# Kernel tuning notes

Measured on AMD Instinct MI355X. Metric: run time of the kernel, lower is better.

## Reference

```python
import jax, jax.numpy as jnp
import numpy as np

N, E = 20000, 320000
NF, EF, GF = 74, 12, 128


def setup_inputs() -> dict:
    key = jax.random.key(0)
    it = iter(jax.random.split(key, 48))
    nrm = lambda shape, s=1.0: jax.random.normal(next(it), shape, jnp.float32) * s
    W = lambda shape: nrm(shape, 0.05)
    d = {}
    d["node_feats"] = nrm((N, NF))
    d["edge_feats"] = nrm((E, EF))
    for k in (1, 2, 3):
        d[f"pn{k}_w"] = W((NF, GF)); d[f"pn{k}_b"] = W((GF,))
        d[f"pe1{k}_w"] = W((NF + EF, GF)); d[f"pe1{k}_b"] = W((GF,))
        d[f"pe2{k}_w"] = W((2 * GF, 1)); d[f"pe2{k}_b"] = W((1,))
        d[f"et{k}_w"] = W((GF, GF)); d[f"et{k}_b"] = W((GF,))
    d["mca_w"] = W((3 * GF, GF)); d["mca_b"] = W((GF,))
    d["mcn_w"] = W((3 * GF, GF)); d["mcn_b"] = W((GF,))
    d["gru_wih"] = W((GF, 3 * GF)); d["gru_whh"] = W((GF, 3 * GF))
    d["gru_bih"] = W((3 * GF,)); d["gru_bhh"] = W((3 * GF,))
    d["src"] = jax.random.randint(next(it), (E,), 0, N, dtype=jnp.int32)
    d["dst"] = jax.random.randint(next(it), (E,), 0, N, dtype=jnp.int32)
    return d


def _forward(node_feats, edge_feats,
             pn1_w, pn1_b, pn2_w, pn2_b, pn3_w, pn3_b,
             pe11_w, pe11_b, pe12_w, pe12_b, pe13_w, pe13_b,
             pe21_w, pe21_b, pe22_w, pe22_b, pe23_w, pe23_b,
             et1_w, et1_b, et2_w, et2_b, et3_w, et3_b,
             mca_w, mca_b, mcn_w, mcn_b,
             gru_wih, gru_whh, gru_bih, gru_bhh,
             src, dst):
    leaky = lambda x: jax.nn.leaky_relu(x, 0.01)
    n_nodes = node_feats.shape[0]
    # projected node features (3 parallel branches), [N, GF]
    hv = [leaky(node_feats @ w + b)
          for w, b in ((pn1_w, pn1_b), (pn2_w, pn2_b), (pn3_w, pn3_b))]
    # apply_edges1: cat(src node feats, raw edge feats) -> [E, NF+EF]
    he1 = jnp.concatenate([node_feats[src], edge_feats], axis=1)
    he1k = [leaky(he1 @ w + b)
            for w, b in ((pe11_w, pe11_b), (pe12_w, pe12_b), (pe13_w, pe13_b))]
    pe2 = ((pe21_w, pe21_b), (pe22_w, pe22_b), (pe23_w, pe23_b))
    et = ((et1_w, et1_b), (et2_w, et2_b), (et3_w, et3_b))

    def edge_softmax(lg):  # softmax over incoming edges per destination node
        m = jax.ops.segment_max(lg, dst, num_segments=n_nodes)
        m = jnp.where(jnp.isfinite(m), m, 0.0)  # guard empty segments
        e = jnp.exp(lg - m[dst])
        s = jax.ops.segment_sum(e, dst, num_segments=n_nodes)
        return e / s[dst]

    ctx = []
    for k in range(3):
        w2, b2 = pe2[k]
        # apply_edges2: cat(dst projected node feats, projected edge feats) -> logits [E,1]
        lg = leaky(jnp.concatenate([hv[k][dst], he1k[k]], axis=1) @ w2 + b2)
        tw, tb = et[k]
        msg = edge_softmax(lg) * (he1k[k] @ tw + tb)  # [E, GF]
        ctx.append(jax.nn.elu(jax.ops.segment_sum(msg, dst, num_segments=n_nodes)))
    context = jnp.concatenate(ctx, axis=1) @ mca_w + mca_b  # [N, GF]
    h = jnp.concatenate(hv, axis=1) @ mcn_w + mcn_b          # [N, GF]
    # torch GRUCell(context, h)
    gi = context @ gru_wih + gru_bih
    gh = h @ gru_whh + gru_bhh
    ir, iz, inn = jnp.split(gi, 3, axis=1)
    hr, hz, hn = jnp.split(gh, 3, axis=1)
    r = jax.nn.sigmoid(ir + hr)
    z = jax.nn.sigmoid(iz + hz)
    n = jnp.tanh(inn + r * hn)
    return jax.nn.relu((1.0 - z) * n + z * h)


def reference(node_feats, edge_feats,
              pn1_w, pn1_b, pn2_w, pn2_b, pn3_w, pn3_b,
              pe11_w, pe11_b, pe12_w, pe12_b, pe13_w, pe13_b,
              pe21_w, pe21_b, pe22_w, pe22_b, pe23_w, pe23_b,
              et1_w, et1_b, et2_w, et2_b, et3_w, et3_b,
              mca_w, mca_b, mcn_w, mcn_b,
              gru_wih, gru_whh, gru_bih, gru_bhh,
              src, dst):
    return _forward(node_feats, edge_feats,
                    pn1_w, pn1_b, pn2_w, pn2_b, pn3_w, pn3_b,
                    pe11_w, pe11_b, pe12_w, pe12_b, pe13_w, pe13_b,
                    pe21_w, pe21_b, pe22_w, pe22_b, pe23_w, pe23_b,
                    et1_w, et1_b, et2_w, et2_b, et3_w, et3_b,
                    mca_w, mca_b, mcn_w, mcn_b,
                    gru_wih, gru_whh, gru_bih, gru_bhh,
                    src, dst)
```

## Files before the change

kernel.cpp:

```cpp
#include <hip/hip_runtime.h>
#include <hip/hip_bf16.h>
#include <math.h>

#define NN 20000
#define EE 320000
#define NFD 74
#define EFD 12

__device__ __forceinline__ float leakyf(float x) { return x > 0.f ? x : 0.01f * x; }
__device__ __forceinline__ float b2f(unsigned short u) {
    union { unsigned int i; float f; } x; x.i = ((unsigned int)u) << 16; return x.f;
}
__device__ __forceinline__ unsigned short f2b(float f) {
    __hip_bfloat16 h = __float2bfloat16(f);
    return *(unsigned short*)&h;
}

typedef __bf16 v8bf __attribute__((ext_vector_type(8)));
typedef float v4f __attribute__((ext_vector_type(4)));
typedef unsigned short us8v __attribute__((ext_vector_type(8)));
union FragU { v8bf v; ushort4 h[2]; };

struct GJob {
    const float* A; const float* B; const float* bias; float* C; const int* cnt;
    int a_off; int c_off; unsigned short* ph;
};

template <int ACT>
__global__ __launch_bounds__(256) void gemm_mfma(
    GJob j0, GJob j1, GJob j2,
    int lda, int ldb, int ldc, int nrows, int K, int M, int split)
{
    GJob jb = (blockIdx.y == 0) ? j0 : ((blockIdx.y == 1) ? j1 : j2);
    const int tiles_m = M >> 7;
    const int tn = blockIdx.x / tiles_m;
    const int tm = blockIdx.x % tiles_m;
    const int n0 = tn << 7, m0 = tm << 7;
    __shared__ __align__(16) unsigned short As[128][40];
    __shared__ __align__(16) unsigned short Bt[128][40];
    const int tid = threadIdx.x;
    const int w = tid >> 6, l = tid & 63;
    const int wr = (w >> 1) * 64, wc = (w & 1) * 64;
    const int fr = l & 15, fg = l >> 4;

    v4f acc[4][4];
#pragma unroll
    for (int ri = 0; ri < 4; ri++)
#pragma unroll
        for (int ci = 0; ci < 4; ci++) {
            acc[ri][ci][0] = 0.f; acc[ri][ci][1] = 0.f;
            acc[ri][ci][2] = 0.f; acc[ri][ci][3] = 0.f;
        }

    for (int k0 = 0; k0 < K; k0 += 32) {
        {
            const int row = tid >> 1, ks = (tid & 1) << 4;
            const int grow = n0 + row;
            const bool rok = grow < nrows;
            const float* Ap = jb.A + (size_t)grow * lda + jb.a_off + k0 + ks;
            unsigned short* dstp = &As[row][ks];
#pragma unroll
            for (int r = 0; r < 16; r += 4) {
                const int gk = k0 + ks + r;
                float4 v = make_float4(0.f, 0.f, 0.f, 0.f);
                if (rok && gk + 3 < K) v = *(const float4*)(Ap + r);
                dstp[r + 0] = f2b(v.x); dstp[r + 1] = f2b(v.y);
                dstp[r + 2] = f2b(v.z); dstp[r + 3] = f2b(v.w);
            }
        }
        {
            const int kk = tid >> 3, cb = (tid & 7) << 4;
            const int gk = k0 + kk;
            const bool kok = gk < K;
            const float* Bp = jb.B + (size_t)gk * ldb + m0 + cb;
#pragma unroll
            for (int r = 0; r < 4; r++) {
                float4 v = make_float4(0.f, 0.f, 0.f, 0.f);
                if (kok) v = *(const float4*)(Bp + r * 4);
                const int c = cb + r * 4;
                Bt[c + 0][kk] = f2b(v.x); Bt[c + 1][kk] = f2b(v.y);
                Bt[c + 2][kk] = f2b(v.z); Bt[c + 3][kk] = f2b(v.w);
            }
        }
        __syncthreads();
        FragU fa[4], fb[4];
#pragma unroll
        for (int ri = 0; ri < 4; ri++) {
            const unsigned short* ap = &As[wr + ri * 16 + fr][0];
            fa[ri].h[0] = *(const ushort4*)(ap + fg * 4);
            fa[ri].h[1] = *(const ushort4*)(ap + 16 + fg * 4);
        }
#pragma unroll
        for (int ci = 0; ci < 4; ci++) {
            const unsigned short* bp = &Bt[wc + ci * 16 + fr][0];
            fb[ci].h[0] = *(const ushort4*)(bp + fg * 4);
            fb[ci].h[1] = *(const ushort4*)(bp + 16 + fg * 4);
        }
#pragma unroll
        for (int ri = 0; ri < 4; ri++)
#pragma unroll
            for (int ci = 0; ci < 4; ci++)
                acc[ri][ci] = __builtin_amdgcn_mfma_f32_16x16x32_bf16(
                    fa[ri].v, fb[ci].v, acc[ri][ci], 0, 0, 0);
        __syncthreads();
    }
#pragma unroll
    for (int ci = 0; ci < 4; ci++) {
        const int gcol = m0 + wc + ci * 16 + fr;
        const float bi = jb.bias[gcol];
        const int gcc = jb.c_off + gcol;
#pragma unroll
        for (int ri = 0; ri < 4; ri++) {
#pragma unroll
            for (int j = 0; j < 4; j++) {
                const int grow = n0 + wr + ri * 16 + fg * 4 + j;
                if (grow >= nrows) continue;
                float v = acc[ri][ci][j] + bi;
                if (ACT == 2) {
                    bool pos = jb.cnt[grow] > 0;
                    v = pos ? (v > 0.f ? v : (__expf(v) - 1.f)) : 0.f;
                }
                if (ACT == 3) {
                    if (gcc < split) v = leakyf(v);
                    else if (jb.ph) jb.ph[(size_t)grow * 384 + (gcc - split)] = f2b(v);
                }
                jb.C[(size_t)grow * ldc + gcc] = v;
            }
        }
    }
}

__global__ void k_pack(
    const float* __restrict__ pn0, const float* __restrict__ pn1, const float* __restrict__ pn2,
    const float* __restrict__ pb0, const float* __restrict__ pb1, const float* __restrict__ pb2,
    const float* __restrict__ pe0, const float* __restrict__ pe1, const float* __restrict__ pe2,
    const float* __restrict__ qb0, const float* __restrict__ qb1, const float* __restrict__ qb2,
    const float* __restrict__ wih, const float* __restrict__ whh,
    float* __restrict__ PK, float* __restrict__ PB, float* __restrict__ WG, float* __restrict__ Z512)
{
    int idx = blockIdx.x * 256 + threadIdx.x;
    const float* pnw[3] = {pn0, pn1, pn2};
    const float* pew[3] = {pe0, pe1, pe2};
    const float* pnb[3] = {pb0, pb1, pb2};
    const float* peb[3] = {qb0, qb1, qb2};
    if (idx < 131072) {
        int r = idx >> 9, c = idx & 511;
        float v;
        if (r < 128) v = (c < 384) ? wih[r * 384 + c] : 0.f;
        else {
            int rr = r - 128;
            if (c < 256) v = whh[rr * 384 + c];
            else if (c < 384) v = 0.f;
            else v = whh[rr * 384 + (c - 128)];
        }
        WG[idx] = v;
    } else if (idx < 131072 + 61440) {
        int t = idx - 131072;
        int r = t / 768, c = t - r * 768;
        int k = (c >> 7) % 3, cc = c & 127;
        PK[t] = (r < NFD) ? ((c < 384) ? pnw[k][r * 128 + cc] : pew[k][r * 128 + cc]) : 0.f;
    } else if (idx < 131072 + 61440 + 768) {
        int c = idx - (131072 + 61440);
        int k = (c >> 7) % 3, cc = c & 127;
        PB[c] = (c < 384) ? pnb[k][cc] : peb[k][cc];
    } else if (idx < 131072 + 61440 + 768 + 512) {
        Z512[idx - (131072 + 61440 + 768)] = 0.f;
    }
}

__global__ void k_prep(const float* __restrict__ nf, float* __restrict__ PA)
{
    int idx = blockIdx.x * 256 + threadIdx.x;
    if (idx < NN * 80) {
        int n = idx / 80, c = idx - n * 80;
        PA[idx] = (c < NFD) ? nf[n * NFD + c] : 0.f;
    }
}

__global__ void k_count(const int* __restrict__ dst, int* __restrict__ cnt)
{
    int e = blockIdx.x * 256 + threadIdx.x;
    if (e < EE) atomicAdd(&cnt[dst[e]], 1);
}

__global__ void k_off(const int* __restrict__ cnt, int* __restrict__ offs,
                      int* __restrict__ cur, int* __restrict__ total)
{
    int n = blockIdx.x * 256 + threadIdx.x;
    if (n < NN) {
        int c = cnt[n];
        int o = atomicAdd(total, c);
        offs[n] = o;
        cur[n] = o;
    }
}

__global__ void k_fill(const int* __restrict__ dst, const int* __restrict__ src,
                       const float* __restrict__ ef,
                       int* __restrict__ cur, int* __restrict__ csr_src,
                       float* __restrict__ EFC)
{
    int e = blockIdx.x * 256 + threadIdx.x;
    if (e < EE) {
        int p = atomicAdd(&cur[dst[e]], 1);
        csr_src[p] = src[e];
        const float4* s = (const float4*)(ef + (size_t)e * 12);
        float4* d = (float4*)(EFC + (size_t)p * 12);
        float4 v0 = s[0], v1 = s[1], v2 = s[2];
        d[0] = v0; d[1] = v1; d[2] = v2;
    }
}

__global__ __launch_bounds__(256) void k_fused(
    const float* __restrict__ HP,
    const unsigned short* __restrict__ PH,
    const float* __restrict__ EFC,
    const float* __restrict__ pw0, const float* __restrict__ pw1, const float* __restrict__ pw2,
    const float* __restrict__ v0, const float* __restrict__ v1, const float* __restrict__ v2,
    const float* __restrict__ b20, const float* __restrict__ b21, const float* __restrict__ b22,
    const int* __restrict__ csr_src,
    const int* __restrict__ offs, const int* __restrict__ cnt,
    float* __restrict__ AX)
{
    const int wid = blockIdx.x * 4 + (threadIdx.x >> 6);
    const int n = wid / 3;
    const int k = wid - n * 3;
    if (n >= NN) return;
    const int lane = threadIdx.x & 63;
    const int er = lane >> 4, cg = lane & 15;
    const int c8 = cg * 8;
    const float* pw = (k == 0) ? pw0 : (k == 1) ? pw1 : pw2;
    const float* vv = (k == 0) ? v0 : (k == 1) ? v1 : v2;
    const float b2 = ((k == 0) ? b20 : (k == 1) ? b21 : b22)[0];
    const float* We = pw + NFD * 128;

    const int o0 = offs[n];
    const int deg = cnt[n];
    float* arow = AX + (size_t)n * 384 + k * 128;
    if (deg == 0) {
        if (er == 0) {
            *(float4*)(arow + c8) = make_float4(0.f, 0.f, 0.f, 0.f);
            *(float4*)(arow + c8 + 4) = make_float4(0.f, 0.f, 0.f, 0.f);
        }
        return;
    }

    float4 wb0 = *(const float4*)(vv + 128 + c8);
    float4 wb1 = *(const float4*)(vv + 128 + c8 + 4);

    float qa;
    {
        float4 wa0 = *(const float4*)(vv + c8);
        float4 wa1 = *(const float4*)(vv + c8 + 4);
        const float* hr = HP + (size_t)n * 768 + k * 128;
        float4 h0 = *(const float4*)(hr + c8);
        float4 h1 = *(const float4*)(hr + c8 + 4);
        qa = h0.x * wa0.x + h0.y * wa0.y + h0.z * wa0.z + h0.w * wa0.w
           + h1.x * wa1.x + h1.y * wa1.y + h1.z * wa1.z + h1.w * wa1.w;
#pragma unroll
        for (int d = 1; d < 16; d <<= 1) qa += __shfl_xor(qa, d, 64);
    }

    const unsigned short* PHk = PH + (size_t)k * 128 + c8;

    int q0 = o0 + ((er < deg) ? er : (deg - 1));
    int sn0 = csr_src[q0];
    const float4* ep0 = (const float4*)(EFC + (size_t)q0 * 12);
    float4 e00 = ep0[0], e01 = ep0[1], e02 = ep0[2];
    int sn1 = sn0;
    float4 e10 = e00, e11 = e01, e12 = e02;
    if (deg > 4) {
        int p1 = 4 + er;
        int q1 = o0 + ((p1 < deg) ? p1 : (deg - 1));
        sn1 = csr_src[q1];
        const float4* ep1 = (const float4*)(EFC + (size_t)q1 * 12);
        e10 = ep1[0]; e11 = ep1[1]; e12 = ep1[2];
    }
    us8v px0 = *(const us8v*)(PHk + (size_t)sn0 * 384);

    float4 a0 = make_float4(0.f, 0.f, 0.f, 0.f);
    float4 a1 = make_float4(0.f, 0.f, 0.f, 0.f);
    float s = 0.f;

    for (int base = 0; base < deg; base += 4) {
        const bool on = (base + er) < deg;
        us8v px1 = px0;
        if (base + 4 < deg) px1 = *(const us8v*)(PHk + (size_t)sn1 * 384);
        int sn2 = sn1;
        float4 e20 = e10, e21 = e11, e22 = e12;
        if (base + 8 < deg) {
            int p2 = base + 8 + er;
            int q2 = o0 + ((p2 < deg) ? p2 : (deg - 1));
            sn2 = csr_src[q2];
            const float4* ep2 = (const float4*)(EFC + (size_t)q2 * 12);
            e20 = ep2[0]; e21 = ep2[1]; e22 = ep2[2];
        }
        float ef[12] = {e00.x, e00.y, e00.z, e00.w, e01.x, e01.y, e01.z, e01.w,
                        e02.x, e02.y, e02.z, e02.w};
        float4 x0 = make_float4(0.f, 0.f, 0.f, 0.f);
        float4 x1 = make_float4(0.f, 0.f, 0.f, 0.f);
#pragma unroll
        for (int j = 0; j < 12; j++) {
            float e = ef[j];
            float4 w0 = *(const float4*)(We + j * 128 + c8);
            float4 w1 = *(const float4*)(We + j * 128 + c8 + 4);
            x0.x += e * w0.x; x0.y += e * w0.y; x0.z += e * w0.z; x0.w += e * w0.w;
            x1.x += e * w1.x; x1.y += e * w1.y; x1.z += e * w1.z; x1.w += e * w1.w;
        }
        x0.x = leakyf(x0.x + b2f(px0[0])); x0.y = leakyf(x0.y + b2f(px0[1]));
        x0.z = leakyf(x0.z + b2f(px0[2])); x0.w = leakyf(x0.w + b2f(px0[3]));
        x1.x = leakyf(x1.x + b2f(px0[4])); x1.y = leakyf(x1.y + b2f(px0[5]));
        x1.z = leakyf(x1.z + b2f(px0[6])); x1.w = leakyf(x1.w + b2f(px0[7]));
        float dd = x0.x * wb0.x + x0.y * wb0.y + x0.z * wb0.z + x0.w * wb0.w
                 + x1.x * wb1.x + x1.y * wb1.y + x1.z * wb1.z + x1.w * wb1.w;
#pragma unroll
        for (int d = 1; d < 16; d <<= 1) dd += __shfl_xor(dd, d, 64);
        float ex = on ? __expf(leakyf(qa + dd + b2)) : 0.f;
        a0.x += ex * x0.x; a0.y += ex * x0.y; a0.z += ex * x0.z; a0.w += ex * x0.w;
        a1.x += ex * x1.x; a1.y += ex * x1.y; a1.z += ex * x1.z; a1.w += ex * x1.w;
        s += ex;
        px0 = px1; sn1 = sn2;
        e00 = e10; e01 = e11; e02 = e12;
        e10 = e20; e11 = e21; e12 = e22;
    }
#pragma unroll
    for (int d = 16; d < 64; d <<= 1) {
        a0.x += __shfl_xor(a0.x, d, 64); a0.y += __shfl_xor(a0.y, d, 64);
        a0.z += __shfl_xor(a0.z, d, 64); a0.w += __shfl_xor(a0.w, d, 64);
        a1.x += __shfl_xor(a1.x, d, 64); a1.y += __shfl_xor(a1.y, d, 64);
        a1.z += __shfl_xor(a1.z, d, 64); a1.w += __shfl_xor(a1.w, d, 64);
        s += __shfl_xor(s, d, 64);
    }
    if (er == 0) {
        float inv = 1.f / s;
        a0.x *= inv; a0.y *= inv; a0.z *= inv; a0.w *= inv;
        a1.x *= inv; a1.y *= inv; a1.z *= inv; a1.w *= inv;
        *(float4*)(arow + c8) = a0;
        *(float4*)(arow + c8 + 4) = a1;
    }
}

__global__ void k_gru2(const float* __restrict__ G, const float* __restrict__ X,
                       const float* __restrict__ bih, const float* __restrict__ bhh,
                       float* __restrict__ out)
{
    int idx = blockIdx.x * 256 + threadIdx.x;
    if (idx >= NN * 128) return;
    int n = idx >> 7, c = idx & 127;
    const float* g = G + (size_t)n * 512;
    float r = 1.f / (1.f + __expf(-(g[c] + bih[c] + bhh[c])));
    float z = 1.f / (1.f + __expf(-(g[128 + c] + bih[128 + c] + bhh[128 + c])));
    float nv = tanhf(g[256 + c] + bih[256 + c] + r * (g[384 + c] + bhh[256 + c]));
    float h = X[(size_t)n * 256 + 128 + c];
    float v = (1.f - z) * nv + z * h;
    out[idx] = v > 0.f ? v : 0.f;
}

extern "C" void kernel_launch(void* const* d_in, const int* in_sizes, int n_in,
                              void* d_out, int out_size, void* d_ws, size_t ws_size,
                              hipStream_t stream)
{
    const float* nf = (const float*)d_in[0];
    const float* ef = (const float*)d_in[1];
    const float *pn_w[3], *pn_b[3], *pe1_w[3], *pe1_b[3], *pe2_w[3], *pe2_b[3], *et_w[3], *et_b[3];
    for (int k = 0; k < 3; k++) {
        int b = 2 + k * 8;
        pn_w[k] = (const float*)d_in[b + 0]; pn_b[k] = (const float*)d_in[b + 1];
        pe1_w[k] = (const float*)d_in[b + 2]; pe1_b[k] = (const float*)d_in[b + 3];
        pe2_w[k] = (const float*)d_in[b + 4]; pe2_b[k] = (const float*)d_in[b + 5];
        et_w[k] = (const float*)d_in[b + 6]; et_b[k] = (const float*)d_in[b + 7];
    }
    const float* mca_w = (const float*)d_in[26]; const float* mca_b = (const float*)d_in[27];
    const float* mcn_w = (const float*)d_in[28]; const float* mcn_b = (const float*)d_in[29];
    const float* wih = (const float*)d_in[30]; const float* whh = (const float*)d_in[31];
    const float* bih = (const float*)d_in[32]; const float* bhh = (const float*)d_in[33];
    const int* src = (const int*)d_in[34];
    const int* dst = (const int*)d_in[35];

    float* W = (float*)d_ws;
    size_t o = 0;
    float* HP = W + o;   o += (size_t)NN * 768;
    float* AX = W + o;   o += (size_t)NN * 384;
    float* EFC = W + o;  o += (size_t)EE * 12;
    float* PK = W + o;   o += 80 * 768;
    float* PB = W + o;   o += 768;
    float* WG = W + o;   o += 256 * 512;
    float* Z512 = W + o; o += 512;
    unsigned short* PHu = (unsigned short*)(W + o); o += (size_t)NN * 192;
    int* cnt = (int*)(W + o);
    int* total = cnt + NN;
    int* offs = total + 1;
    int* cur = offs + NN;
    int* csr_src = cur + NN;
    size_t need = o * 4 + (size_t)(NN * 3 + 1 + EE) * 4;
    if (ws_size < need) return;

    float* PA = EFC;
    float* Xb = AX;
    float* Gb = HP;

    hipMemsetAsync(cnt, 0, (NN + 1) * sizeof(int), stream);

    dim3 blk(256);
    k_pack<<<757, blk, 0, stream>>>(
        pn_w[0], pn_w[1], pn_w[2], pn_b[0], pn_b[1], pn_b[2],
        pe1_w[0], pe1_w[1], pe1_w[2], pe1_b[0], pe1_b[1], pe1_b[2],
        wih, whh, PK, PB, WG, Z512);
    k_prep<<<(NN * 80 + 255) / 256, blk, 0, stream>>>(nf, PA);

    const int rt = (NN + 127) / 128;

    {
        GJob j = {PA, PK, PB, HP, nullptr, 0, 0, PHu};
        gemm_mfma<3><<<dim3(rt * 6, 1), blk, 0, stream>>>(j, j, j, 80, 768, 768, NN, 80, 768, 384);
    }

    k_count<<<(EE + 255) / 256, blk, 0, stream>>>(dst, cnt);
    k_off<<<(NN + 255) / 256, blk, 0, stream>>>(cnt, offs, cur, total);
    k_fill<<<(EE + 255) / 256, blk, 0, stream>>>(dst, src, ef, cur, csr_src, EFC);

    k_fused<<<dim3((NN * 3) / 4), blk, 0, stream>>>(HP, PHu, EFC,
        pe1_w[0], pe1_w[1], pe1_w[2], pe2_w[0], pe2_w[1], pe2_w[2],
        pe2_b[0], pe2_b[1], pe2_b[2], csr_src, offs, cnt, AX);

    {
        GJob j0 = {AX, et_w[0], et_b[0], HP, cnt, 0 * 128, 384 + 0 * 128, nullptr};
        GJob j1 = {AX, et_w[1], et_b[1], HP, cnt, 1 * 128, 384 + 1 * 128, nullptr};
        GJob j2 = {AX, et_w[2], et_b[2], HP, cnt, 2 * 128, 384 + 2 * 128, nullptr};
        gemm_mfma<2><<<dim3(rt, 3), blk, 0, stream>>>(j0, j1, j2, 384, 128, 768, NN, 128, 128, 0);
    }
    {
        GJob j0 = {HP, mca_w, mca_b, Xb, nullptr, 384, 0, nullptr};
        GJob j1 = {HP, mcn_w, mcn_b, Xb, nullptr, 0, 128, nullptr};
        gemm_mfma<0><<<dim3(rt, 2), blk, 0, stream>>>(j0, j1, j1, 768, 128, 256, NN, 384, 128, 0);
    }
    {
        GJob j = {Xb, WG, Z512, Gb, nullptr, 0, 0, nullptr};
        gemm_mfma<0><<<dim3(rt * 4, 1), blk, 0, stream>>>(j, j, j, 256, 512, 512, NN, 256, 512, 0);
    }

    k_gru2<<<(NN * 128 + 255) / 256, blk, 0, stream>>>(Gb, Xb, bih, bhh, (float*)d_out);
}
```

Measured before the change: 529.6 us.

## Store intermediates and pre-transposed weights as bf16 to halve GEMM traffic

All GEMM operands are now bf16. Weights are packed once into transposed bf16 layouts, and activations (HP, AX, X) are written as bf16 by their producers. This lets the GEMM tile loads become plain 16-byte copies with no fp32-to-bf16 conversion or transposed scatter into shared memory, and it halves intermediate memory traffic. The fused edge kernel reads the unified bf16 HP buffer and writes bf16 output. Its block mapping is also reordered by branch, and the workspace aliasing is reorganised. The cost is slightly more rounding in the intermediates and a larger pack kernel.

```diff
diff --git a/kernel.cpp b/kernel.cpp
--- a/kernel.cpp
+++ b/kernel.cpp
@@ -22,14 +22,18 @@
 union FragU { v8bf v; ushort4 h[2]; };
 
 struct GJob {
-    const float* A; const float* B; const float* bias; float* C; const int* cnt;
-    int a_off; int c_off; unsigned short* ph;
+    const unsigned short* A;
+    const unsigned short* B;
+    const float* bias;
+    float* C;
+    unsigned short* Ch;
+    const int* cnt;
+    int lda; int a_off; int ldc; int ldch; int c_off;
 };
 
 template <int ACT>
-__global__ __launch_bounds__(256) void gemm_mfma(
-    GJob j0, GJob j1, GJob j2,
-    int lda, int ldb, int ldc, int nrows, int K, int M, int split)
+__global__ __launch_bounds__(256) void gemm_bf(
+    GJob j0, GJob j1, GJob j2, int nrows, int K, int M, int split)
 {
     GJob jb = (blockIdx.y == 0) ? j0 : ((blockIdx.y == 1) ? j1 : j2);
     const int tiles_m = M >> 7;
@@ -37,7 +41,7 @@
     const int tm = blockIdx.x % tiles_m;
     const int n0 = tn << 7, m0 = tm << 7;
     __shared__ __align__(16) unsigned short As[128][40];
-    __shared__ __align__(16) unsigned short Bt[128][40];
+    __shared__ __align__(16) unsigned short Bs[128][40];
     const int tid = threadIdx.x;
     const int w = tid >> 6, l = tid & 63;
     const int wr = (w >> 1) * 64, wc = (w & 1) * 64;
@@ -52,35 +56,25 @@
             acc[ri][ci][2] = 0.f; acc[ri][ci][3] = 0.f;
         }
 
+    const int row = tid >> 1, half = tid & 1;
+
     for (int k0 = 0; k0 < K; k0 += 32) {
+        const int kb = k0 + half * 16;
+        const bool kok = kb < K;
         {
-            const int row = tid >> 1, ks = (tid & 1) << 4;
-            const int grow = n0 + row;
-            const bool rok = grow < nrows;
-            const float* Ap = jb.A + (size_t)grow * lda + jb.a_off + k0 + ks;
-            unsigned short* dstp = &As[row][ks];
-#pragma unroll
-            for (int r = 0; r < 16; r += 4) {
-                const int gk = k0 + ks + r;
-                float4 v = make_float4(0.f, 0.f, 0.f, 0.f);
-                if (rok && gk + 3 < K) v = *(const float4*)(Ap + r);
-                dstp[r + 0] = f2b(v.x); dstp[r + 1] = f2b(v.y);
-                dstp[r + 2] = f2b(v.z); dstp[r + 3] = f2b(v.w);
-            }
+            const bool rok = kok && (n0 + row) < nrows;
+            const unsigned short* Ap = jb.A + (size_t)(n0 + row) * jb.lda + jb.a_off + kb;
+            uint4 v0 = make_uint4(0, 0, 0, 0), v1 = v0;
+            if (rok) { v0 = *(const uint4*)Ap; v1 = *(const uint4*)(Ap + 8); }
+            *(uint4*)&As[row][half * 16] = v0;
+            *(uint4*)&As[row][half * 16 + 8] = v1;
         }
         {
-            const int kk = tid >> 3, cb = (tid & 7) << 4;
-            const int gk = k0 + kk;
-            const bool kok = gk < K;
-            const float* Bp = jb.B + (size_t)gk * ldb + m0 + cb;
-#pragma unroll
-            for (int r = 0; r < 4; r++) {
-                float4 v = make_float4(0.f, 0.f, 0.f, 0.f);
-                if (kok) v = *(const float4*)(Bp + r * 4);
-                const int c = cb + r * 4;
-                Bt[c + 0][kk] = f2b(v.x); Bt[c + 1][kk] = f2b(v.y);
-                Bt[c + 2][kk] = f2b(v.z); Bt[c + 3][kk] = f2b(v.w);
-            }
+            const unsigned short* Bp = jb.B + (size_t)(m0 + row) * K + kb;
+            uint4 v0 = make_uint4(0, 0, 0, 0), v1 = v0;
+            if (kok) { v0 = *(const uint4*)Bp; v1 = *(const uint4*)(Bp + 8); }
+            *(uint4*)&Bs[row][half * 16] = v0;
+            *(uint4*)&Bs[row][half * 16 + 8] = v1;
         }
         __syncthreads();
         FragU fa[4], fb[4];
@@ -92,7 +86,7 @@
         }
 #pragma unroll
         for (int ci = 0; ci < 4; ci++) {
-            const unsigned short* bp = &Bt[wc + ci * 16 + fr][0];
+            const unsigned short* bp = &Bs[wc + ci * 16 + fr][0];
             fb[ci].h[0] = *(const ushort4*)(bp + fg * 4);
             fb[ci].h[1] = *(const ushort4*)(bp + 16 + fg * 4);
         }
@@ -109,42 +103,57 @@
         const int gcol = m0 + wc + ci * 16 + fr;
         const float bi = jb.bias[gcol];
         const int gcc = jb.c_off + gcol;
+        const bool lk = (ACT == 3) && (gcc < split);
 #pragma unroll
         for (int ri = 0; ri < 4; ri++) {
 #pragma unroll
-            for (int j = 0; j < 4; j++) {
-                const int grow = n0 + wr + ri * 16 + fg * 4 + j;
+            for (int jj = 0; jj < 4; jj++) {
+                const int grow = n0 + wr + ri * 16 + fg * 4 + jj;
                 if (grow >= nrows) continue;
-                float v = acc[ri][ci][j] + bi;
+                float v = acc[ri][ci][jj] + bi;
                 if (ACT == 2) {
                     bool pos = jb.cnt[grow] > 0;
                     v = pos ? (v > 0.f ? v : (__expf(v) - 1.f)) : 0.f;
                 }
-                if (ACT == 3) {
-                    if (gcc < split) v = leakyf(v);
-                    else if (jb.ph) jb.ph[(size_t)grow * 384 + (gcc - split)] = f2b(v);
-                }
-                jb.C[(size_t)grow * ldc + gcc] = v;
+                if (ACT == 3 && lk) v = leakyf(v);
+                if (jb.C)  jb.C[(size_t)grow * jb.ldc + gcc] = v;
+                if (jb.Ch) jb.Ch[(size_t)grow * jb.ldch + gcc] = f2b(v);
             }
         }
     }
 }
 
+#define SZ_PKT 61440
+#define SZ_WGT 131072
+#define SZ_ETT 49152
+#define SZ_MCT 98304
 __global__ void k_pack(
     const float* __restrict__ pn0, const float* __restrict__ pn1, const float* __restrict__ pn2,
     const float* __restrict__ pb0, const float* __restrict__ pb1, const float* __restrict__ pb2,
     const float* __restrict__ pe0, const float* __restrict__ pe1, const float* __restrict__ pe2,
     const float* __restrict__ qb0, const float* __restrict__ qb1, const float* __restrict__ qb2,
     const float* __restrict__ wih, const float* __restrict__ whh,
-    float* __restrict__ PK, float* __restrict__ PB, float* __restrict__ WG, float* __restrict__ Z512)
+    const float* __restrict__ et0, const float* __restrict__ et1, const float* __restrict__ et2,
+    const float* __restrict__ mca, const float* __restrict__ mcn,
+    unsigned short* __restrict__ PKt, unsigned short* __restrict__ WGt,
+    unsigned short* __restrict__ ETt, unsigned short* __restrict__ MCt,
+    float* __restrict__ PB, float* __restrict__ Z512)
 {
     int idx = blockIdx.x * 256 + threadIdx.x;
     const float* pnw[3] = {pn0, pn1, pn2};
     const float* pew[3] = {pe0, pe1, pe2};
     const float* pnb[3] = {pb0, pb1, pb2};
     const float* peb[3] = {qb0, qb1, qb2};
-    if (idx < 131072) {
-        int r = idx >> 9, c = idx & 511;
+    const float* etw[3] = {et0, et1, et2};
+    if (idx < SZ_PKT) {
+        int c = idx / 80, r = idx - c * 80;
+        int k = (c >> 7) % 3, cc = c & 127;
+        float v = 0.f;
+        if (r < NFD) v = (c < 384) ? pnw[k][r * 128 + cc] : pew[k][r * 128 + cc];
+        PKt[idx] = f2b(v);
+    } else if (idx < SZ_PKT + SZ_WGT) {
+        int t = idx - SZ_PKT;
+        int c = t >> 8, r = t & 255;
         float v;
         if (r < 128) v = (c < 384) ? wih[r * 384 + c] : 0.f;
         else {
@@ -153,27 +162,32 @@
             else if (c < 384) v = 0.f;
             else v = whh[rr * 384 + (c - 128)];
         }
-        WG[idx] = v;
-    } else if (idx < 131072 + 61440) {
-        int t = idx - 131072;
-        int r = t / 768, c = t - r * 768;
-        int k = (c >> 7) % 3, cc = c & 127;
-        PK[t] = (r < NFD) ? ((c < 384) ? pnw[k][r * 128 + cc] : pew[k][r * 128 + cc]) : 0.f;
-    } else if (idx < 131072 + 61440 + 768) {
-        int c = idx - (131072 + 61440);
+        WGt[t] = f2b(v);
+    } else if (idx < SZ_PKT + SZ_WGT + SZ_ETT) {
+        int t = idx - (SZ_PKT + SZ_WGT);
+        int k = t / 16384, rem = t - k * 16384;
+        int c = rem >> 7, r = rem & 127;
+        ETt[t] = f2b(etw[k][r * 128 + c]);
+    } else if (idx < SZ_PKT + SZ_WGT + SZ_ETT + SZ_MCT) {
+        int t = idx - (SZ_PKT + SZ_WGT + SZ_ETT);
+        int m = t / 49152, rem = t - m * 49152;
+        int c = rem / 384, r = rem - c * 384;
+        MCt[t] = f2b((m == 0 ? mca : mcn)[r * 128 + c]);
+    } else if (idx < SZ_PKT + SZ_WGT + SZ_ETT + SZ_MCT + 768) {
+        int c = idx - (SZ_PKT + SZ_WGT + SZ_ETT + SZ_MCT);
         int k = (c >> 7) % 3, cc = c & 127;
         PB[c] = (c < 384) ? pnb[k][cc] : peb[k][cc];
-    } else if (idx < 131072 + 61440 + 768 + 512) {
-        Z512[idx - (131072 + 61440 + 768)] = 0.f;
-    }
-}
-
-__global__ void k_prep(const float* __restrict__ nf, float* __restrict__ PA)
+    } else if (idx < SZ_PKT + SZ_WGT + SZ_ETT + SZ_MCT + 768 + 512) {
+        Z512[idx - (SZ_PKT + SZ_WGT + SZ_ETT + SZ_MCT + 768)] = 0.f;
+    }
+}
+
+__global__ void k_prep(const float* __restrict__ nf, unsigned short* __restrict__ PA)
 {
     int idx = blockIdx.x * 256 + threadIdx.x;
     if (idx < NN * 80) {
         int n = idx / 80, c = idx - n * 80;
-        PA[idx] = (c < NFD) ? nf[n * NFD + c] : 0.f;
+        PA[idx] = f2b((c < NFD) ? nf[n * NFD + c] : 0.f);
     }
 }
 
@@ -212,20 +226,17 @@
 }
 
 __global__ __launch_bounds__(256) void k_fused(
-    const float* __restrict__ HP,
-    const unsigned short* __restrict__ PH,
+    const unsigned short* __restrict__ HPh,
     const float* __restrict__ EFC,
     const float* __restrict__ pw0, const float* __restrict__ pw1, const float* __restrict__ pw2,
     const float* __restrict__ v0, const float* __restrict__ v1, const float* __restrict__ v2,
     const float* __restrict__ b20, const float* __restrict__ b21, const float* __restrict__ b22,
     const int* __restrict__ csr_src,
     const int* __restrict__ offs, const int* __restrict__ cnt,
-    float* __restrict__ AX)
-{
-    const int wid = blockIdx.x * 4 + (threadIdx.x >> 6);
-    const int n = wid / 3;
-    const int k = wid - n * 3;
-    if (n >= NN) return;
+    unsigned short* __restrict__ AXh)
+{
+    const int k = blockIdx.x / (NN / 4);
+    const int n = (blockIdx.x - k * (NN / 4)) * 4 + (threadIdx.x >> 6);
     const int lane = threadIdx.x & 63;
     const int er = lane >> 4, cg = lane & 15;
     const int c8 = cg * 8;
@@ -236,11 +247,13 @@
 
     const int o0 = offs[n];
     const int deg = cnt[n];
-    float* arow = AX + (size_t)n * 384 + k * 128;
+    unsigned short* arow = AXh + (size_t)n * 384 + k * 128 + c8;
     if (deg == 0) {
         if (er == 0) {
-            *(float4*)(arow + c8) = make_float4(0.f, 0.f, 0.f, 0.f);
-            *(float4*)(arow + c8 + 4) = make_float4(0.f, 0.f, 0.f, 0.f);
+            us8v z;
+#pragma unroll
+            for (int i = 0; i < 8; i++) z[i] = 0;
+            *(us8v*)arow = z;
         }
         return;
     }
@@ -252,16 +265,14 @@
     {
         float4 wa0 = *(const float4*)(vv + c8);
         float4 wa1 = *(const float4*)(vv + c8 + 4);
-        const float* hr = HP + (size_t)n * 768 + k * 128;
-        float4 h0 = *(const float4*)(hr + c8);
-        float4 h1 = *(const float4*)(hr + c8 + 4);
-        qa = h0.x * wa0.x + h0.y * wa0.y + h0.z * wa0.z + h0.w * wa0.w
-           + h1.x * wa1.x + h1.y * wa1.y + h1.z * wa1.z + h1.w * wa1.w;
+        us8v h8 = *(const us8v*)(HPh + (size_t)n * 768 + k * 128 + c8);
+        qa = b2f(h8[0]) * wa0.x + b2f(h8[1]) * wa0.y + b2f(h8[2]) * wa0.z + b2f(h8[3]) * wa0.w
+           + b2f(h8[4]) * wa1.x + b2f(h8[5]) * wa1.y + b2f(h8[6]) * wa1.z + b2f(h8[7]) * wa1.w;
 #pragma unroll
         for (int d = 1; d < 16; d <<= 1) qa += __shfl_xor(qa, d, 64);
     }
 
-    const unsigned short* PHk = PH + (size_t)k * 128 + c8;
+    const unsigned short* PHk = HPh + 384 + (size_t)k * 128 + c8;
 
     int q0 = o0 + ((er < deg) ? er : (deg - 1));
     int sn0 = csr_src[q0];
@@ -276,7 +287,7 @@
         const float4* ep1 = (const float4*)(EFC + (size_t)q1 * 12);
         e10 = ep1[0]; e11 = ep1[1]; e12 = ep1[2];
     }
-    us8v px0 = *(const us8v*)(PHk + (size_t)sn0 * 384);
+    us8v px0 = *(const us8v*)(PHk + (size_t)sn0 * 768);
 
     float4 a0 = make_float4(0.f, 0.f, 0.f, 0.f);
     float4 a1 = make_float4(0.f, 0.f, 0.f, 0.f);
@@ -285,7 +296,7 @@
     for (int base = 0; base < deg; base += 4) {
         const bool on = (base + er) < deg;
         us8v px1 = px0;
-        if (base + 4 < deg) px1 = *(const us8v*)(PHk + (size_t)sn1 * 384);
+        if (base + 4 < deg) px1 = *(const us8v*)(PHk + (size_t)sn1 * 768);
         int sn2 = sn1;
         float4 e20 = e10, e21 = e11, e22 = e12;
         if (base + 8 < deg) {
@@ -333,10 +344,12 @@
     }
     if (er == 0) {
         float inv = 1.f / s;
-        a0.x *= inv; a0.y *= inv; a0.z *= inv; a0.w *= inv;
-        a1.x *= inv; a1.y *= inv; a1.z *= inv; a1.w *= inv;
-        *(float4*)(arow + c8) = a0;
-        *(float4*)(arow + c8 + 4) = a1;
+        us8v outv;
+        outv[0] = f2b(a0.x * inv); outv[1] = f2b(a0.y * inv);
+        outv[2] = f2b(a0.z * inv); outv[3] = f2b(a0.w * inv);
+        outv[4] = f2b(a1.x * inv); outv[5] = f2b(a1.y * inv);
+        outv[6] = f2b(a1.z * inv); outv[7] = f2b(a1.w * inv);
+        *(us8v*)arow = outv;
     }
 }
 
@@ -379,65 +392,70 @@
 
     float* W = (float*)d_ws;
     size_t o = 0;
-    float* HP = W + o;   o += (size_t)NN * 768;
-    float* AX = W + o;   o += (size_t)NN * 384;
-    float* EFC = W + o;  o += (size_t)EE * 12;
-    float* PK = W + o;   o += 80 * 768;
-    float* PB = W + o;   o += 768;
-    float* WG = W + o;   o += 256 * 512;
-    float* Z512 = W + o; o += 512;
-    unsigned short* PHu = (unsigned short*)(W + o); o += (size_t)NN * 192;
+    float* Xb = W + o;                                  o += (size_t)NN * 256;
+    unsigned short* HPh = (unsigned short*)(W + o);     o += (size_t)NN * 384;
+    unsigned short* Xh  = (unsigned short*)(W + o);     o += (size_t)NN * 128;
+    unsigned short* PKt = (unsigned short*)(W + o);     o += SZ_PKT / 2;
+    unsigned short* WGt = (unsigned short*)(W + o);     o += SZ_WGT / 2;
+    unsigned short* ETt = (unsigned short*)(W + o);     o += SZ_ETT / 2;
+    unsigned short* MCt = (unsigned short*)(W + o);     o += SZ_MCT / 2;
+    float* PB = W + o;                                  o += 768;
+    float* Z512 = W + o;                                o += 512;
     int* cnt = (int*)(W + o);
     int* total = cnt + NN;
     int* offs = total + 1;
     int* cur = offs + NN;
-    int* csr_src = cur + NN;
-    size_t need = o * 4 + (size_t)(NN * 3 + 1 + EE) * 4;
+    int* csr_src = cur + NN;                            o += (size_t)3 * NN + 1 + EE;
+    float* G = W + o;
+    unsigned short* AXh = (unsigned short*)G;
+    float* EFC = G + (size_t)NN * 192;
+    unsigned short* PA = (unsigned short*)EFC;
+    size_t gspan = (size_t)NN * 512;
+    size_t espan = (size_t)NN * 192 + (size_t)EE * 12;
+    o += (gspan > espan) ? gspan : espan;
+    size_t need = o * 4;
     if (ws_size < need) return;
 
-    float* PA = EFC;
-    float* Xb = AX;
-    float* Gb = HP;
-
     hipMemsetAsync(cnt, 0, (NN + 1) * sizeof(int), stream);
 
     dim3 blk(256);
-    k_pack<<<757, blk, 0, stream>>>(
+    k_pack<<<(SZ_PKT + SZ_WGT + SZ_ETT + SZ_MCT + 768 + 512 + 255) / 256, blk, 0, stream>>>(
         pn_w[0], pn_w[1], pn_w[2], pn_b[0], pn_b[1], pn_b[2],
         pe1_w[0], pe1_w[1], pe1_w[2], pe1_b[0], pe1_b[1], pe1_b[2],
-        wih, whh, PK, PB, WG, Z512);
+        wih, whh, et_w[0], et_w[1], et_w[2], mca_w, mcn_w,
+        PKt, WGt, ETt, MCt, PB, Z512);
     k_prep<<<(NN * 80 + 255) / 256, blk, 0, stream>>>(nf, PA);
 
     const int rt = (NN + 127) / 128;
 
     {
-        GJob j = {PA, PK, PB, HP, nullptr, 0, 0, PHu};
-        gemm_mfma<3><<<dim3(rt * 6, 1), blk, 0, stream>>>(j, j, j, 80, 768, 768, NN, 80, 768, 384);
+        GJob j = {PA, PKt, PB, nullptr, HPh, nullptr, 80, 0, 0, 768, 0};
+        gemm_bf<3><<<dim3(rt * 6, 1), blk, 0, stream>>>(j, j, j, NN, 80, 768, 384);
     }
 
     k_count<<<(EE + 255) / 256, blk, 0, stream>>>(dst, cnt);
     k_off<<<(NN + 255) / 256, blk, 0, stream>>>(cnt, offs, cur, total);
     k_fill<<<(EE + 255) / 256, blk, 0, stream>>>(dst, src, ef, cur, csr_src, EFC);
 
-    k_fused<<<dim3((NN * 3) / 4), blk, 0, stream>>>(HP, PHu, EFC,
+    k_fused<<<dim3((NN / 4) * 3), blk, 0, stream>>>(HPh, EFC,
         pe1_w[0], pe1_w[1], pe1_w[2], pe2_w[0], pe2_w[1], pe2_w[2],
-        pe2_b[0], pe2_b[1], pe2_b[2], csr_src, offs, cnt, AX);
+        pe2_b[0], pe2_b[1], pe2_b[2], csr_src, offs, cnt, AXh);
 
     {
-        GJob j0 = {AX, et_w[0], et_b[0], HP, cnt, 0 * 128, 384 + 0 * 128, nullptr};
-        GJob j1 = {AX, et_w[1], et_b[1], HP, cnt, 1 * 128, 384 + 1 * 128, nullptr};
-        GJob j2 = {AX, et_w[2], et_b[2], HP, cnt, 2 * 128, 384 + 2 * 128, nullptr};
-        gemm_mfma<2><<<dim3(rt, 3), blk, 0, stream>>>(j0, j1, j2, 384, 128, 768, NN, 128, 128, 0);
+        GJob j0 = {AXh, ETt,             et_b[0], nullptr, HPh, cnt, 384, 0,   0, 768, 384};
+        GJob j1 = {AXh, ETt + 16384,     et_b[1], nullptr, HPh, cnt, 384, 128, 0, 768, 512};
+        GJob j2 = {AXh, ETt + 32768,     et_b[2], nullptr, HPh, cnt, 384, 256, 0, 768, 640};
+        gemm_bf<2><<<dim3(rt, 3), blk, 0, stream>>>(j0, j1, j2, NN, 128, 128, 0);
     }
     {
-        GJob j0 = {HP, mca_w, mca_b, Xb, nullptr, 384, 0, nullptr};
-        GJob j1 = {HP, mcn_w, mcn_b, Xb, nullptr, 0, 128, nullptr};
-        gemm_mfma<0><<<dim3(rt, 2), blk, 0, stream>>>(j0, j1, j1, 768, 128, 256, NN, 384, 128, 0);
+        GJob j0 = {HPh, MCt,         mca_b, Xb, Xh, nullptr, 768, 384, 256, 256, 0};
+        GJob j1 = {HPh, MCt + 49152, mcn_b, Xb, Xh, nullptr, 768, 0,   256, 256, 128};
+        gemm_bf<0><<<dim3(rt, 2), blk, 0, stream>>>(j0, j1, j1, NN, 384, 128, 0);
     }
     {
-        GJob j = {Xb, WG, Z512, Gb, nullptr, 0, 0, nullptr};
-        gemm_mfma<0><<<dim3(rt * 4, 1), blk, 0, stream>>>(j, j, j, 256, 512, 512, NN, 256, 512, 0);
-    }
-
-    k_gru2<<<(NN * 128 + 255) / 256, blk, 0, stream>>>(Gb, Xb, bih, bhh, (float*)d_out);
-}
+        GJob j = {Xh, WGt, Z512, G, nullptr, nullptr, 256, 0, 512, 0, 0};
+        gemm_bf<0><<<dim3(rt * 4, 1), blk, 0, stream>>>(j, j, j, NN, 256, 512, 0);
+    }
+
+    k_gru2<<<(NN * 128 + 255) / 256, blk, 0, stream>>>(G, Xb, bih, bhh, (float*)d_out);
+}
```

Result: faster. 493.0 us (-6.9%).
